# Optimization experiments

Measured on AMD Instinct MI355X. Metric: run time of the kernel, lower is better.

Reference implementation:

```python
import jax, jax.numpy as jnp
import numpy as np

ROTARY_BASE = 10000
INFTY_APPROX = 1e30
B, T, M, H, D = 2, 2048, 2048, 16, 128


def rope(x):
    # x: [B, T, H, D]; half-split rotary encoding
    *_, length, _, width = x.shape
    half = width // 2
    positions = jnp.arange(length, dtype=jnp.float32)[None, :, None, None]      # [1,T,1,1]
    dims = jnp.arange(half, dtype=jnp.float32)
    ang_freqs = jnp.power(float(ROTARY_BASE), -dims / half)[None, None, None, :]  # [1,1,1,D/2]
    radians = positions * ang_freqs
    cos = jnp.cos(radians).astype(x.dtype)
    sin = jnp.sin(radians).astype(x.dtype)
    even, odd = x[..., :half], x[..., half:]
    r_even = even * cos - odd * sin
    r_odd = even * sin + odd * cos
    return jnp.concatenate([r_even, r_odd], axis=-1)


def setup_inputs() -> dict:
    key = jax.random.key(0)
    k0, k1, k2, k3, k4 = jax.random.split(key, 5)
    return {
        "x": jax.random.normal(k0, (B, T, M), dtype=jnp.float32),
        "w_aq": jax.random.normal(k1, (H, M, D), dtype=jnp.float32) * (M ** -0.5),
        "w_ak": jax.random.normal(k2, (H, M, D), dtype=jnp.float32) * (M ** -0.5),
        "w_av": jax.random.normal(k3, (H, M, D), dtype=jnp.float32) * (M ** -0.5),
        "w_ao": jax.random.normal(k4, (H, D, M), dtype=jnp.float32) * ((2 * 24 * M) ** -0.5),
    }


def reference(x, w_aq, w_ak, w_av, w_ao):
    q = jnp.einsum("btm,hmd->bthd", x, w_aq)
    k = jnp.einsum("btm,hmd->bthd", x, w_ak)
    v = jnp.einsum("btm,hmd->bthd", x, w_av)
    q = rope(q)
    k = rope(k)
    # muP attention scaling: 1/d_head (not 1/sqrt(d_head))
    mult = (1.0 / D) ** 0.5
    s = jnp.einsum("bihd,bjhd->bhij", mult * q, mult * k)  # [B,H,T,T]
    i = jnp.arange(T)[:, None]
    j = jnp.arange(T)[None, :]
    mask = (i < j)[None, None, :, :]  # mask future positions
    s = s - jnp.asarray(INFTY_APPROX, dtype=x.dtype) * mask
    p = jax.nn.softmax(s, axis=-1)
    o = jnp.einsum("bhij,bjhd->bihd", p, v)
    r = jnp.einsum("bihd,hdm->bim", o, w_ao)
    return r
```

## Files before the change

kernel.cpp:

```cpp
#include <hip/hip_runtime.h>

#define Bb 2
#define Tt 2048
#define Mm 2048
#define Hh 16
#define Dd 128

typedef __attribute__((ext_vector_type(8))) short bf16x8;
typedef __attribute__((ext_vector_type(4))) float f32x4;
typedef __attribute__((ext_vector_type(16))) float f32x16;

__device__ __forceinline__ unsigned short f2bf(float f) {
    unsigned int u = __builtin_bit_cast(unsigned int, f);
    u += 0x7FFFu + ((u >> 16) & 1u);
    return (unsigned short)(u >> 16);
}

__device__ __forceinline__ unsigned int cvt_pk_bf16(float lo, float hi) {
    unsigned int r;
    asm("v_cvt_pk_bf16_f32 %0, %1, %2" : "=v"(r) : "v"(lo), "v"(hi));
    return r;
}

__device__ __forceinline__ float fexp2(float x) { return __builtin_amdgcn_exp2f(x); }

__device__ __forceinline__ void gld16(const void* g, void* l) {
    __builtin_amdgcn_global_load_lds(
        (const __attribute__((address_space(1))) void*)g,
        (__attribute__((address_space(3))) void*)l, 16, 0, 0);
}


__global__ __launch_bounds__(256) void cvt_x2(const float* __restrict__ x,
                                              unsigned short* __restrict__ xb2) {
    const int blk = blockIdx.x;
    const int mt = blk >> 5, kt = blk & 31;
#pragma unroll
    for (int it = 0; it < 4; ++it) {
        int s = it * 256 + threadIdx.x;
        int row = ((s >> 6) & 3) * 32 + (s & 31);
        int k = (s >> 8) * 16 + ((s >> 5) & 1) * 8;
        const float* sp = x + ((long)(mt * 128 + row)) * 2048 + kt * 64 + k;
        float4 a = *(const float4*)sp;
        float4 b = *(const float4*)(sp + 4);
        uint4 pk;
        pk.x = (unsigned int)f2bf(a.x) | ((unsigned int)f2bf(a.y) << 16);
        pk.y = (unsigned int)f2bf(a.z) | ((unsigned int)f2bf(a.w) << 16);
        pk.z = (unsigned int)f2bf(b.x) | ((unsigned int)f2bf(b.y) << 16);
        pk.w = (unsigned int)f2bf(b.z) | ((unsigned int)f2bf(b.w) << 16);
        *(uint4*)(xb2 + (((long)(mt * 32 + kt)) * 1024 + s) * 8) = pk;
    }
}

__global__ __launch_bounds__(256) void w_qkv_tile(
    const float* __restrict__ wq, const float* __restrict__ wk, const float* __restrict__ wv,
    unsigned short* __restrict__ outBase) {
    __shared__ float tile[64][132];
    const int kt = blockIdx.x;
    const int zy = blockIdx.y;
    const int which = zy >> 4, head = zy & 15;
    const float* src = (which == 0 ? wq : which == 1 ? wk : wv) + (long)head * 2048 * 128;
    const int tid = threadIdx.x;
#pragma unroll
    for (int it = 0; it < 8; ++it) {
        int f = it * 256 + tid;
        int row = f >> 5, c4 = f & 31;
        float4 v = *(const float4*)(src + (long)(kt * 64 + row) * 128 + c4 * 4);
        tile[row][c4 * 4 + 0] = v.x;
        tile[row][c4 * 4 + 1] = v.y;
        tile[row][c4 * 4 + 2] = v.z;
        tile[row][c4 * 4 + 3] = v.w;
    }
    __syncthreads();
    const int ntile = head >> 1, wn = head & 1;
    unsigned short* outp = outBase + (long)which * 4194304 +
                           ((long)(ntile * 32 + kt)) * 2048 * 8;
#pragma unroll
    for (int it = 0; it < 4; ++it) {
        int up = it * 256 + tid;
        int kk = up >> 8, nf = (up >> 6) & 3, l = up & 63;
        int il = l & 31, hl = l >> 5;
        int d = il + 64 * (nf & 1) + 32 * (nf >> 1);
        int kl = kk * 16 + hl * 8;
        uint4 pk;
        pk.x = (unsigned int)f2bf(tile[kl + 0][d]) | ((unsigned int)f2bf(tile[kl + 1][d]) << 16);
        pk.y = (unsigned int)f2bf(tile[kl + 2][d]) | ((unsigned int)f2bf(tile[kl + 3][d]) << 16);
        pk.z = (unsigned int)f2bf(tile[kl + 4][d]) | ((unsigned int)f2bf(tile[kl + 5][d]) << 16);
        pk.w = (unsigned int)f2bf(tile[kl + 6][d]) | ((unsigned int)f2bf(tile[kl + 7][d]) << 16);
        int u = kk * 512 + (wn * 4 + nf) * 64 + l;
        *(uint4*)(outp + (long)u * 8) = pk;
    }
}

__global__ __launch_bounds__(256) void transpose_cvt(const float* __restrict__ in,
                                                     unsigned short* __restrict__ out,
                                                     int rows, int cols,
                                                     long in_slab, long out_slab) {
    __shared__ float tile[32][33];
    const float* ip = in + (long)blockIdx.z * in_slab;
    unsigned short* op = out + (long)blockIdx.z * out_slab;
    int r0 = blockIdx.x * 32, c0 = blockIdx.y * 32;
    int tx = threadIdx.x & 31, ty = threadIdx.x >> 5;
#pragma unroll
    for (int j = 0; j < 32; j += 8)
        tile[ty + j][tx] = ip[(long)(r0 + ty + j) * cols + c0 + tx];
    __syncthreads();
#pragma unroll
    for (int j = 0; j < 32; j += 8)
        op[(long)(c0 + ty + j) * rows + r0 + tx] = f2bf(tile[tx][ty + j]);
}

__global__ __launch_bounds__(256) void rope_tab(float* __restrict__ cosT,
                                                float* __restrict__ sinT) {
    int idx = blockIdx.x * 256 + threadIdx.x;
    int t = idx >> 6, d = idx & 63;
    float freq = powf(10000.f, -(float)d / 64.f);
    float ang = (float)t * freq;
    sinT[idx] = sinf(ang);
    cosT[idx] = cosf(ang);
}

__global__ __launch_bounds__(256, 2) void proj_gemm4(
    const unsigned short* __restrict__ xb2,
    const unsigned short* __restrict__ wT2,
    unsigned short* __restrict__ qO,
    unsigned short* __restrict__ kO,
    unsigned short* __restrict__ vtO,
    const float* __restrict__ cosT,
    const float* __restrict__ sinT) {
    __shared__ __align__(16) char lds[49152];
    const int bm = blockIdx.x;
    const int bn = blockIdx.y;
    const int mode = bn >> 3, ntile = bn & 7;
    const unsigned short* Asrc = xb2 + ((long)bm * 32) * 1024 * 8;
    const unsigned short* Bsrc = wT2 + (long)mode * 4194304 + ((long)ntile * 32) * 2048 * 8;

    const int tid = threadIdx.x, lane = tid & 63, wave = tid >> 6;
    const int il = lane & 31, hl = lane >> 5;
    const int wm = wave >> 1, wn = wave & 1;

    f32x16 acc[2][4];
#pragma unroll
    for (int a = 0; a < 2; ++a)
#pragma unroll
        for (int b2 = 0; b2 < 4; ++b2)
#pragma unroll
            for (int e = 0; e < 16; ++e) acc[a][b2][e] = 0.f;

    for (int kt = 0; kt < 32; ++kt) {
#pragma unroll
        for (int l = 0; l < 4; ++l) {
            int s = l * 256 + tid;
            gld16(Asrc + ((long)kt * 1024 + s) * 8, lds + s * 16);
        }
#pragma unroll
        for (int l = 0; l < 8; ++l) {
            int u = l * 256 + tid;
            gld16(Bsrc + ((long)kt * 2048 + u) * 8, lds + 16384 + u * 16);
        }
        asm volatile("s_waitcnt vmcnt(0)" ::: "memory");
        __builtin_amdgcn_s_barrier();

#pragma unroll
        for (int kk = 0; kk < 4; ++kk) {
            bf16x8 af[2], bf[4];
#pragma unroll
            for (int mf = 0; mf < 2; ++mf)
                af[mf] = *(const bf16x8*)(lds + (kk * 256 + (wm * 2 + mf) * 64 + lane) * 16);
#pragma unroll
            for (int nf = 0; nf < 4; ++nf)
                bf[nf] = *(const bf16x8*)(lds + 16384 + (kk * 512 + (wn * 4 + nf) * 64 + lane) * 16);
            __builtin_amdgcn_s_setprio(1);
#pragma unroll
            for (int mf = 0; mf < 2; ++mf)
#pragma unroll
                for (int nf = 0; nf < 4; ++nf)
                    acc[mf][nf] = __builtin_amdgcn_mfma_f32_32x32x16_bf16(af[mf], bf[nf], acc[mf][nf], 0, 0, 0);
            __builtin_amdgcn_s_setprio(0);
        }
        asm volatile("" ::: "memory");
        __builtin_amdgcn_s_barrier();
    }

    const int b = bm >> 4;
    const int t0 = (bm & 15) * 128;
    const int head = ntile * 2 + wn;

    if (mode < 2) {
        const float qs = (mode == 0) ? 0.011271055f : 1.0f;
        unsigned short* outp = (mode == 0) ? qO : kO;
        long hb = ((long)(b * Hh + head)) * Tt;
#pragma unroll
        for (int mf = 0; mf < 2; ++mf)
#pragma unroll
            for (int np = 0; np < 2; ++np) {
                int d_lo = il + 32 * np;
#pragma unroll
                for (int reg = 0; reg < 16; ++reg) {
                    int r = (reg & 3) + 8 * (reg >> 2) + 4 * hl;
                    int t = t0 + wm * 64 + mf * 32 + r;
                    float c = cosT[t * 64 + d_lo], s = sinT[t * 64 + d_lo];
                    float ev = acc[mf][np * 2][reg], od = acc[mf][np * 2 + 1][reg];
                    long base = (hb + t) * Dd;
                    outp[base + d_lo]      = f2bf((ev * c - od * s) * qs);
                    outp[base + d_lo + 64] = f2bf((ev * s + od * c) * qs);
                }
            }
    } else {
        char* patch = lds + wave * 8192;
        long hdbase = ((long)(b * Hh + head)) * Dd;
#pragma unroll
        for (int mf = 0; mf < 2; ++mf) {
#pragma unroll
            for (int nf = 0; nf < 4; ++nf) {
                int dslot = nf * 32 + il;
                int swz = (dslot & 3) << 4;
#pragma unroll
                for (int qg = 0; qg < 4; ++qg) {
                    uint2 w;
                    w.x = cvt_pk_bf16(acc[mf][nf][qg * 4 + 0], acc[mf][nf][qg * 4 + 1]);
                    w.y = cvt_pk_bf16(acc[mf][nf][qg * 4 + 2], acc[mf][nf][qg * 4 + 3]);
                    *(uint2*)(patch + dslot * 64 + ((qg * 16 + hl * 8) ^ swz)) = w;
                }
            }
            __builtin_amdgcn_s_waitcnt(0);
#pragma unroll
            for (int p = 0; p < 8; ++p) {
                int dslot = p * 16 + (lane >> 2);
                int t8 = lane & 3;
                uint4 v = *(const uint4*)(patch + dslot * 64 + ((t8 * 16) ^ ((dslot & 3) << 4)));
                int ordv = dslot >> 5, il2 = dslot & 31;
                int d = il2 + 32 * (ordv >> 1) + 64 * (ordv & 1);
                int tg = t0 + wm * 64 + mf * 32 + t8 * 8;
                *(uint4*)(vtO + (hdbase + d) * Tt + tg) = v;
            }
            __builtin_amdgcn_s_waitcnt(0);
        }
    }
}

__global__ __launch_bounds__(256) void attn_kernel(
    const unsigned short* __restrict__ q,
    const unsigned short* __restrict__ k,
    const unsigned short* __restrict__ vt,
    unsigned short* __restrict__ o) {
    __shared__ __align__(16) unsigned short lds[32768];

    const int lid = (int)blockIdx.x;
    const int p = lid & 255;
    const int bh = p & 31;
    const int q0 = p >> 5;
    const int qb = (lid >> 8) ? (15 - q0) : q0;

    const int tid = threadIdx.x, lane = tid & 63, wave = tid >> 6;
    const int h = lane >> 5, iln = lane & 31;

    const unsigned short* qp = q + (long)bh * Tt * Dd;
    const unsigned short* kp = k + (long)bh * Tt * Dd;
    const unsigned short* vp = vt + (long)bh * Dd * Tt;

    const int i_g = qb * 128 + wave * 32 + iln;
    bf16x8 qf[8];
#pragma unroll
    for (int kk = 0; kk < 8; ++kk)
        qf[kk] = *(const bf16x8*)(qp + (long)i_g * Dd + kk * 16 + h * 8);

    f32x16 accO[4];
#pragma unroll
    for (int nb = 0; nb < 4; ++nb)
#pragma unroll
        for (int e = 0; e < 16; ++e) accO[nb][e] = 0.f;

    float m_r = -1e30f, l_r = 0.f;
    const int ntiles = 2 * qb + 2;

    auto stage = [&](int buf, int tix) {
        const int j0s = tix * 64;
#pragma unroll
        for (int it = 0; it < 4; ++it) {
            int f = it * 256 + tid;
            int rk = f >> 4, ck = f & 15;
            gld16(kp + ((long)(j0s + rk) * Dd + ((ck ^ (rk & 7)) << 3)),
                  (char*)lds + buf * 16384 + f * 16);
            int rv = f >> 3, cv = f & 7;
            gld16(vp + ((long)rv * Tt + j0s + ((cv ^ (rv & 7)) << 3)),
                  (char*)lds + 32768 + buf * 16384 + f * 16);
        }
    };

    stage(0, 0);

    for (int tix = 0; tix < ntiles; ++tix) {
        const int cur = tix & 1;
        const int j0 = tix * 64;
        if (tix + 1 < ntiles) {
            stage(cur ^ 1, tix + 1);
            asm volatile("s_waitcnt vmcnt(8)" ::: "memory");
        } else {
            asm volatile("s_waitcnt vmcnt(0)" ::: "memory");
        }
        __builtin_amdgcn_s_barrier();

        const char* Kb = (const char*)lds + cur * 16384;
        const char* Vb = (const char*)lds + 32768 + cur * 16384;

        f32x16 sacc[2];
#pragma unroll
        for (int mb = 0; mb < 2; ++mb)
#pragma unroll
            for (int e = 0; e < 16; ++e) sacc[mb][e] = 0.f;

        __builtin_amdgcn_s_setprio(1);
#pragma unroll
        for (int mb = 0; mb < 2; ++mb) {
            int row = mb * 32 + iln;
            const char* Kr = Kb + row * 256;
            int sw = row & 7;
#pragma unroll
            for (int kk = 0; kk < 8; ++kk) {
                bf16x8 kf = *(const bf16x8*)(Kr + 16 * ((kk * 2 + h) ^ sw));
                sacc[mb] = __builtin_amdgcn_mfma_f32_32x32x16_bf16(kf, qf[kk], sacc[mb], 0, 0, 0);
            }
        }
        __builtin_amdgcn_s_setprio(0);

        const bool domask = (j0 + 63 > qb * 128);
        if (domask) {
#pragma unroll
            for (int mb = 0; mb < 2; ++mb)
#pragma unroll
                for (int reg = 0; reg < 16; ++reg) {
                    int j = j0 + mb * 32 + (reg & 3) + 8 * (reg >> 2) + 4 * h;
                    if (j > i_g) sacc[mb][reg] = -1e30f;
                }
        }

        float red[16];
#pragma unroll
        for (int r = 0; r < 16; ++r) red[r] = fmaxf(sacc[0][r], sacc[1][r]);
#pragma unroll
        for (int s = 8; s >= 1; s >>= 1)
#pragma unroll
            for (int r = 0; r < s; ++r) red[r] = fmaxf(red[r], red[r + s]);
        float mx = fmaxf(red[0], __shfl_xor(red[0], 32, 64));

        if (__any(mx > m_r + 8.f)) {
            float mn = fmaxf(m_r, mx);
            float corr = fexp2(m_r - mn);
            m_r = mn;
            l_r *= corr;
#pragma unroll
            for (int reg = 0; reg < 16; ++reg) {
                int rrow = (reg & 3) + 8 * (reg >> 2) + 4 * h;
                float c = __shfl(corr, rrow, 64);
#pragma unroll
                for (int nb = 0; nb < 4; ++nb) accO[nb][reg] *= c;
            }
        }

        float pe[2][16];
#pragma unroll
        for (int mb = 0; mb < 2; ++mb)
#pragma unroll
            for (int r = 0; r < 16; ++r) pe[mb][r] = fexp2(sacc[mb][r] - m_r);
        float sr[16];
#pragma unroll
        for (int r = 0; r < 16; ++r) sr[r] = pe[0][r] + pe[1][r];
#pragma unroll
        for (int s = 8; s >= 1; s >>= 1)
#pragma unroll
            for (int r = 0; r < s; ++r) sr[r] += sr[r + s];
        l_r += sr[0] + __shfl_xor(sr[0], 32, 64);

        unsigned int pu[2][8];
#pragma unroll
        for (int mb = 0; mb < 2; ++mb)
#pragma unroll
            for (int t = 0; t < 8; ++t)
                pu[mb][t] = cvt_pk_bf16(pe[mb][2 * t], pe[mb][2 * t + 1]);

        unsigned int rv2[2][4];
#pragma unroll
        for (int mb = 0; mb < 2; ++mb)
#pragma unroll
            for (int u = 0; u < 4; ++u) {
                unsigned int sv = h ? pu[mb][(u & 1) + 4 * (u >> 1)]
                                    : pu[mb][2 + (u & 1) + 4 * (u >> 1)];
                rv2[mb][u] = __shfl_xor(sv, 32, 64);
            }

        __builtin_amdgcn_s_setprio(1);
#pragma unroll
        for (int kk2 = 0; kk2 < 4; ++kk2) {
            const int mb = kk2 >> 1, c2 = kk2 & 1;
            unsigned int w0 = h ? rv2[mb][2 * c2 + 0] : pu[mb][4 * c2 + 0];
            unsigned int w1 = h ? rv2[mb][2 * c2 + 1] : pu[mb][4 * c2 + 1];
            unsigned int w2 = h ? pu[mb][4 * c2 + 2] : rv2[mb][2 * c2 + 0];
            unsigned int w3 = h ? pu[mb][4 * c2 + 3] : rv2[mb][2 * c2 + 1];
            uint4 aw; aw.x = w0; aw.y = w1; aw.z = w2; aw.w = w3;
            bf16x8 af = __builtin_bit_cast(bf16x8, aw);
#pragma unroll
            for (int nb = 0; nb < 4; ++nb) {
                int d = nb * 32 + iln;
                int byte = d * 128 + 16 * ((kk2 * 2 + h) ^ (d & 7));
                bf16x8 vf = *(const bf16x8*)(Vb + byte);
                accO[nb] = __builtin_amdgcn_mfma_f32_32x32x16_bf16(af, vf, accO[nb], 0, 0, 0);
            }
        }
        __builtin_amdgcn_s_setprio(0);

        asm volatile("" ::: "memory");
        __builtin_amdgcn_s_barrier();
    }

    const int b = bh >> 4, hh = bh & 15;
    float invl = 1.f / l_r;
#pragma unroll
    for (int reg = 0; reg < 16; ++reg) {
        int rrow = (reg & 3) + 8 * (reg >> 2) + 4 * h;
        float iv = __shfl(invl, rrow, 64);
        int t = qb * 128 + wave * 32 + rrow;
        long base = ((long)(b * Tt + t) * Hh + hh) * Dd;
#pragma unroll
        for (int nb = 0; nb < 4; ++nb)
            o[base + nb * 32 + iln] = f2bf(accO[nb][reg] * iv);
    }
}

__global__ __launch_bounds__(256) void out_gemm(
    const unsigned short* __restrict__ oIn,
    const unsigned short* __restrict__ woT,
    float* __restrict__ out) {
    __shared__ __align__(16) unsigned short smem[32768];
    const int bm = blockIdx.x, bn = blockIdx.y;
    const int tid = threadIdx.x;
    const int lane = tid & 63;
    const int wave = tid >> 6;
    const int g = lane >> 4;
    const int ln = lane & 15;

    const unsigned short* arow = oIn + (long)bm * 128 * Mm;
    const unsigned short* brow = woT + (long)bn * 128 * Mm;

    f32x4 acc[2][8];
#pragma unroll
    for (int a = 0; a < 2; ++a)
#pragma unroll
        for (int b2 = 0; b2 < 8; ++b2)
#pragma unroll
            for (int e = 0; e < 4; ++e) acc[a][b2][e] = 0.f;

    auto stage = [&](int buf, int kt) {
        const int k0 = kt * 64;
#pragma unroll
        for (int it = 0; it < 4; ++it) {
            int f = it * 256 + tid;
            int r = f >> 3, c = f & 7;
            long off = (long)r * Mm + k0 + ((c ^ (r & 7)) << 3);
            gld16(arow + off, (char*)smem + buf * 32768 + f * 16);
            gld16(brow + off, (char*)smem + buf * 32768 + 16384 + f * 16);
        }
    };

    stage(0, 0);

    for (int kt = 0; kt < Mm / 64; ++kt) {
        const int cur = kt & 1;
        if (kt + 1 < Mm / 64) {
            stage(cur ^ 1, kt + 1);
            asm volatile("s_waitcnt vmcnt(8)" ::: "memory");
        } else {
            asm volatile("s_waitcnt vmcnt(0)" ::: "memory");
        }
        __builtin_amdgcn_s_barrier();

        const char* Ab = (const char*)smem + cur * 32768;
        const char* Bv = Ab + 16384;
#pragma unroll
        for (int kc = 0; kc < 2; ++kc) {
            bf16x8 af[2];
#pragma unroll
            for (int rf = 0; rf < 2; ++rf) {
                int row = wave * 32 + rf * 16 + ln;
                int byte = (row * 128 + kc * 64 + g * 16) ^ ((row & 7) << 4);
                af[rf] = *(const bf16x8*)(Ab + byte);
            }
#pragma unroll
            for (int ni = 0; ni < 8; ++ni) {
                int row = ni * 16 + ln;
                int byte = (row * 128 + kc * 64 + g * 16) ^ ((row & 7) << 4);
                bf16x8 bfv = *(const bf16x8*)(Bv + byte);
#pragma unroll
                for (int rf = 0; rf < 2; ++rf)
                    acc[rf][ni] = __builtin_amdgcn_mfma_f32_16x16x32_bf16(af[rf], bfv, acc[rf][ni], 0, 0, 0);
            }
        }
        asm volatile("" ::: "memory");
        __builtin_amdgcn_s_barrier();
    }

#pragma unroll
    for (int rf = 0; rf < 2; ++rf)
#pragma unroll
        for (int reg = 0; reg < 4; ++reg) {
            long row = bm * 128 + wave * 32 + rf * 16 + g * 4 + reg;
#pragma unroll
            for (int ni = 0; ni < 8; ++ni)
                out[row * Mm + bn * 128 + ni * 16 + ln] = acc[rf][ni][reg];
        }
}


extern "C" void kernel_launch(void* const* d_in, const int* in_sizes, int n_in,
                              void* d_out, int out_size, void* d_ws, size_t ws_size,
                              hipStream_t stream) {
    const float* x    = (const float*)d_in[0];
    const float* w_aq = (const float*)d_in[1];
    const float* w_ak = (const float*)d_in[2];
    const float* w_av = (const float*)d_in[3];
    const float* w_ao = (const float*)d_in[4];
    float* out = (float*)d_out;

    char* ws = (char*)d_ws;
    const long SZ_BTM = 16777216;
    const long SZ_W   = 8388608;
    unsigned short* xb2 = (unsigned short*)(ws);
    unsigned short* qB  = (unsigned short*)(ws + SZ_BTM);
    unsigned short* kB  = (unsigned short*)(ws + 2 * SZ_BTM);
    unsigned short* vtB = (unsigned short*)(ws + 3 * SZ_BTM);
    unsigned short* oB  = (unsigned short*)(ws + 4 * SZ_BTM);
    unsigned short* wT2 = (unsigned short*)(ws + 5 * SZ_BTM);
    unsigned short* woT = (unsigned short*)(ws + 5 * SZ_BTM + 3 * SZ_W);
    float* cosT = (float*)(ws + 5 * SZ_BTM + 4 * SZ_W);
    float* sinT = (float*)(ws + 5 * SZ_BTM + 4 * SZ_W + 524288);

    cvt_x2<<<1024, 256, 0, stream>>>(x, xb2);
    w_qkv_tile<<<dim3(32, 48), 256, 0, stream>>>(w_aq, w_ak, w_av, wT2);
    transpose_cvt<<<dim3(64, 64, 1), 256, 0, stream>>>(w_ao, woT, 2048, 2048, 0, 0);
    rope_tab<<<512, 256, 0, stream>>>(cosT, sinT);

    proj_gemm4<<<dim3(32, 24), 256, 0, stream>>>(xb2, wT2, qB, kB, vtB, cosT, sinT);
    attn_kernel<<<dim3(512), 256, 0, stream>>>(qB, kB, vtB, oB);
    out_gemm<<<dim3(32, 16), 256, 0, stream>>>(oB, woT, out);
}
```

Measured before the change: 267.9 us.

## Double-buffer LDS in QKV projection GEMM with half-size k-steps

The projection GEMM now splits each 64-wide k-tile into two halves and double-buffers them in LDS (two 24 KB buffers), issuing the next stage's global loads before waiting on the current one with a partial vmcnt. The aim is to overlap global-to-LDS traffic with MFMA work instead of serialising load then compute. Launch bounds are raised to 3 blocks per CU to allow more occupancy. The trailing barrier must still protect buffer reuse, and the higher occupancy target may add register pressure.

```diff
diff --git a/kernel.cpp b/kernel.cpp
--- a/kernel.cpp
+++ b/kernel.cpp
@@ -120,7 +120,7 @@
     cosT[idx] = cosf(ang);
 }
 
-__global__ __launch_bounds__(256, 2) void proj_gemm4(
+__global__ __launch_bounds__(256, 3) void proj_gemm5(
     const unsigned short* __restrict__ xb2,
     const unsigned short* __restrict__ wT2,
     unsigned short* __restrict__ qO,
@@ -147,29 +147,45 @@
 #pragma unroll
             for (int e = 0; e < 16; ++e) acc[a][b2][e] = 0.f;
 
-    for (int kt = 0; kt < 32; ++kt) {
+    auto stage = [&](int buf, int kt2) {
+        const int kt = kt2 >> 1, hf = kt2 & 1;
+        const unsigned short* A0 = Asrc + ((long)kt * 1024 + hf * 512) * 8;
+        const unsigned short* B0 = Bsrc + ((long)kt * 2048 + hf * 1024) * 8;
+        char* dst = lds + buf * 24576;
+#pragma unroll
+        for (int l = 0; l < 2; ++l) {
+            int s = l * 256 + tid;
+            gld16(A0 + (long)s * 8, dst + s * 16);
+        }
 #pragma unroll
         for (int l = 0; l < 4; ++l) {
-            int s = l * 256 + tid;
-            gld16(Asrc + ((long)kt * 1024 + s) * 8, lds + s * 16);
-        }
-#pragma unroll
-        for (int l = 0; l < 8; ++l) {
             int u = l * 256 + tid;
-            gld16(Bsrc + ((long)kt * 2048 + u) * 8, lds + 16384 + u * 16);
-        }
-        asm volatile("s_waitcnt vmcnt(0)" ::: "memory");
+            gld16(B0 + (long)u * 8, dst + 8192 + u * 16);
+        }
+    };
+
+    stage(0, 0);
+
+    for (int kt2 = 0; kt2 < 64; ++kt2) {
+        const int cur = kt2 & 1;
+        if (kt2 + 1 < 64) {
+            stage(cur ^ 1, kt2 + 1);
+            asm volatile("s_waitcnt vmcnt(6)" ::: "memory");
+        } else {
+            asm volatile("s_waitcnt vmcnt(0)" ::: "memory");
+        }
         __builtin_amdgcn_s_barrier();
 
-#pragma unroll
-        for (int kk = 0; kk < 4; ++kk) {
+        const char* bc = lds + cur * 24576;
+#pragma unroll
+        for (int kk2 = 0; kk2 < 2; ++kk2) {
             bf16x8 af[2], bf[4];
 #pragma unroll
             for (int mf = 0; mf < 2; ++mf)
-                af[mf] = *(const bf16x8*)(lds + (kk * 256 + (wm * 2 + mf) * 64 + lane) * 16);
+                af[mf] = *(const bf16x8*)(bc + (kk2 * 256 + (wm * 2 + mf) * 64 + lane) * 16);
 #pragma unroll
             for (int nf = 0; nf < 4; ++nf)
-                bf[nf] = *(const bf16x8*)(lds + 16384 + (kk * 512 + (wn * 4 + nf) * 64 + lane) * 16);
+                bf[nf] = *(const bf16x8*)(bc + 8192 + (kk2 * 512 + (wn * 4 + nf) * 64 + lane) * 16);
             __builtin_amdgcn_s_setprio(1);
 #pragma unroll
             for (int mf = 0; mf < 2; ++mf)
@@ -539,7 +555,7 @@
     transpose_cvt<<<dim3(64, 64, 1), 256, 0, stream>>>(w_ao, woT, 2048, 2048, 0, 0);
     rope_tab<<<512, 256, 0, stream>>>(cosT, sinT);
 
-    proj_gemm4<<<dim3(32, 24), 256, 0, stream>>>(xb2, wT2, qB, kB, vtB, cosT, sinT);
+    proj_gemm5<<<dim3(32, 24), 256, 0, stream>>>(xb2, wT2, qB, kB, vtB, cosT, sinT);
     attn_kernel<<<dim3(512), 256, 0, stream>>>(qB, kB, vtB, oB);
     out_gemm<<<dim3(32, 16), 256, 0, stream>>>(oB, woT, out);
 }
```

Measured after the change: 265.9 us. No clear change (-0.7%).

## Restructure QKV projection GEMM into 512-thread blocks with triple-buffered pipelined loads

Applied to the files above, without the earlier changes.

The QKV projection kernel is rewritten to use 512-thread blocks covering 256 rows. Each block handles a 384-column slice as one wide 256-column sub-GEMM followed by one narrow 128-column sub-GEMM, which gives a 16x16 grid of 256 blocks. The main loop now uses a three-slot LDS ring with split half-stage prefetch and partial vmcnt waits, so global loads overlap with MFMA work instead of waiting on a full drain each k-step. The weight pre-tiling layout is changed to per-head contiguous segments to match. The aim is to raise data reuse per block, cut the tail-wave imbalance, and hide load latency, at the cost of more LDS, more barriers, and a more complex schedule.

```diff
diff --git a/kernel.cpp b/kernel.cpp
--- a/kernel.cpp
+++ b/kernel.cpp
@@ -72,9 +72,7 @@
         tile[row][c4 * 4 + 3] = v.w;
     }
     __syncthreads();
-    const int ntile = head >> 1, wn = head & 1;
-    unsigned short* outp = outBase + (long)which * 4194304 +
-                           ((long)(ntile * 32 + kt)) * 2048 * 8;
+    unsigned short* outp = outBase + (((long)(which * 16 + head)) * 32 + kt) * 1024 * 8;
 #pragma unroll
     for (int it = 0; it < 4; ++it) {
         int up = it * 256 + tid;
@@ -87,8 +85,7 @@
         pk.y = (unsigned int)f2bf(tile[kl + 2][d]) | ((unsigned int)f2bf(tile[kl + 3][d]) << 16);
         pk.z = (unsigned int)f2bf(tile[kl + 4][d]) | ((unsigned int)f2bf(tile[kl + 5][d]) << 16);
         pk.w = (unsigned int)f2bf(tile[kl + 6][d]) | ((unsigned int)f2bf(tile[kl + 7][d]) << 16);
-        int u = kk * 512 + (wn * 4 + nf) * 64 + l;
-        *(uint4*)(outp + (long)u * 8) = pk;
+        *(uint4*)(outp + (long)up * 8) = pk;
     }
 }
 
@@ -120,7 +117,191 @@
     cosT[idx] = cosf(ang);
 }
 
-__global__ __launch_bounds__(256, 2) void proj_gemm4(
+template <bool WIDE>
+__device__ __forceinline__ void proj_sub(
+    const unsigned short* __restrict__ xb2,
+    const unsigned short* __restrict__ wT2,
+    char* lds, int bm, int offc,
+    unsigned short* __restrict__ qO, unsigned short* __restrict__ kO,
+    unsigned short* __restrict__ vtO,
+    const float* __restrict__ cosT, const float* __restrict__ sinT, int tid) {
+    const int lane = tid & 63, wave = tid >> 6;
+    const int il = lane & 31, hl = lane >> 5;
+    const int wm = WIDE ? (wave >> 2) : (wave >> 1);
+    const int wn = WIDE ? (wave & 3) : (wave & 1);
+    const int hseg0 = offc >> 7;
+    const int mode = offc >> 11;
+    constexpr int MF = WIDE ? 4 : 2;
+
+    f32x16 acc[MF][2];
+#pragma unroll
+    for (int a = 0; a < MF; ++a)
+#pragma unroll
+        for (int b2 = 0; b2 < 2; ++b2)
+#pragma unroll
+            for (int e = 0; e < 16; ++e) acc[a][b2][e] = 0.f;
+
+    auto stage = [&](int buf, int t, int half) {
+        const int kt = t >> 1, hf = t & 1;
+        char* dst = lds + buf * 32768;
+        if (WIDE) {
+#pragma unroll
+            for (int i = 0; i < 2; ++i) {
+                int f = (half * 2 + i) * 512 + tid;
+                if (f < 1024) {
+                    int kk = f >> 9, rf = (f >> 6) & 7, l = f & 63;
+                    int mt = 2 * bm + (rf >> 2), rb = rf & 3;
+                    gld16(xb2 + (((long)(mt * 32 + kt)) * 1024 + (2 * hf + kk) * 256 + rb * 64 + l) * 8,
+                          dst + f * 16);
+                } else {
+                    int g = f - 1024;
+                    int kk = g >> 9, cf = (g >> 6) & 7, l = g & 63;
+                    int hs = hseg0 + (cf >> 2), nf = cf & 3;
+                    gld16(wT2 + (((long)(hs * 32 + kt)) * 1024 + (2 * hf + kk) * 256 + nf * 64 + l) * 8,
+                          dst + 16384 + g * 16);
+                }
+            }
+        } else {
+            const int i0 = half ? 2 : 0, i1 = half ? 3 : 2;
+            for (int i = i0; i < i1; ++i) {
+                int f = i * 512 + tid;
+                if (f < 1024) {
+                    int kk = f >> 9, rf = (f >> 6) & 7, l = f & 63;
+                    int mt = 2 * bm + (rf >> 2), rb = rf & 3;
+                    gld16(xb2 + (((long)(mt * 32 + kt)) * 1024 + (2 * hf + kk) * 256 + rb * 64 + l) * 8,
+                          dst + f * 16);
+                } else {
+                    int g = f - 1024;
+                    int kk = g >> 8, nf = (g >> 6) & 3, l = g & 63;
+                    gld16(wT2 + (((long)(hseg0 * 32 + kt)) * 1024 + (2 * hf + kk) * 256 + nf * 64 + l) * 8,
+                          dst + 16384 + g * 16);
+                }
+            }
+        }
+    };
+
+    stage(0, 0, 0); stage(0, 0, 1);
+    stage(1, 1, 0); stage(1, 1, 1);
+
+    int cur = 0;
+    for (int t = 0; t < 64; ++t) {
+        int pre = cur + 2; if (pre >= 3) pre -= 3;
+        const char* bc = lds + cur * 32768;
+
+        if (t + 2 < 64) {
+            stage(pre, t + 2, 0);
+            if (WIDE) asm volatile("s_waitcnt vmcnt(6)" ::: "memory");
+            else      asm volatile("s_waitcnt vmcnt(5)" ::: "memory");
+        } else if (t == 62) {
+            if (WIDE) asm volatile("s_waitcnt vmcnt(4)" ::: "memory");
+            else      asm volatile("s_waitcnt vmcnt(3)" ::: "memory");
+        } else {
+            asm volatile("s_waitcnt vmcnt(0)" ::: "memory");
+        }
+        asm volatile("s_barrier" ::: "memory");
+        {
+            bf16x8 af[MF], bf[2];
+#pragma unroll
+            for (int mf = 0; mf < MF; ++mf)
+                af[mf] = *(const bf16x8*)(bc + ((wm * MF + mf) * 64 + lane) * 16);
+#pragma unroll
+            for (int nf = 0; nf < 2; ++nf)
+                bf[nf] = *(const bf16x8*)(bc + 16384 + ((wn * 2 + nf) * 64 + lane) * 16);
+            asm volatile("s_waitcnt lgkmcnt(0)" ::: "memory");
+            __builtin_amdgcn_s_setprio(1);
+#pragma unroll
+            for (int mf = 0; mf < MF; ++mf)
+#pragma unroll
+                for (int nf = 0; nf < 2; ++nf)
+                    acc[mf][nf] = __builtin_amdgcn_mfma_f32_32x32x16_bf16(af[mf], bf[nf], acc[mf][nf], 0, 0, 0);
+            __builtin_amdgcn_s_setprio(0);
+        }
+        asm volatile("s_barrier" ::: "memory");
+
+        if (t + 2 < 64) stage(pre, t + 2, 1);
+        asm volatile("s_barrier" ::: "memory");
+        {
+            constexpr int BO = WIDE ? 512 : 256;
+            bf16x8 af[MF], bf[2];
+#pragma unroll
+            for (int mf = 0; mf < MF; ++mf)
+                af[mf] = *(const bf16x8*)(bc + (512 + (wm * MF + mf) * 64 + lane) * 16);
+#pragma unroll
+            for (int nf = 0; nf < 2; ++nf)
+                bf[nf] = *(const bf16x8*)(bc + 16384 + (BO + (wn * 2 + nf) * 64 + lane) * 16);
+            asm volatile("s_waitcnt lgkmcnt(0)" ::: "memory");
+            __builtin_amdgcn_s_setprio(1);
+#pragma unroll
+            for (int mf = 0; mf < MF; ++mf)
+#pragma unroll
+                for (int nf = 0; nf < 2; ++nf)
+                    acc[mf][nf] = __builtin_amdgcn_mfma_f32_32x32x16_bf16(af[mf], bf[nf], acc[mf][nf], 0, 0, 0);
+            __builtin_amdgcn_s_setprio(0);
+        }
+        asm volatile("s_barrier" ::: "memory");
+        cur = (cur == 2) ? 0 : cur + 1;
+    }
+    asm volatile("s_waitcnt vmcnt(0)" ::: "memory");
+    __syncthreads();
+
+    const int b = bm >> 3;
+    const int t0 = (bm & 7) * 256;
+    const int head_g = WIDE ? (hseg0 + (wn >> 1)) : hseg0;
+    const int head_l = head_g & 15;
+    const int opar = WIDE ? (wn & 1) : wn;
+    constexpr int WMS = WIDE ? 128 : 64;
+
+    if (mode < 2) {
+        const float qs = (mode == 0) ? 0.011271055f : 1.0f;
+        unsigned short* outp = (mode == 0) ? qO : kO;
+        long hb = ((long)(b * Hh + head_l)) * Tt;
+        int d_lo = il + 32 * opar;
+#pragma unroll
+        for (int mf = 0; mf < MF; ++mf)
+#pragma unroll
+            for (int reg = 0; reg < 16; ++reg) {
+                int r = (reg & 3) + 8 * (reg >> 2) + 4 * hl;
+                int tt = t0 + wm * WMS + mf * 32 + r;
+                float c = cosT[tt * 64 + d_lo], s = sinT[tt * 64 + d_lo];
+                float ev = acc[mf][0][reg], od = acc[mf][1][reg];
+                long base = (hb + tt) * Dd;
+                outp[base + d_lo]      = f2bf((ev * c - od * s) * qs);
+                outp[base + d_lo + 64] = f2bf((ev * s + od * c) * qs);
+            }
+    } else {
+        char* patch = lds + wave * 4096;
+        long hdbase = ((long)(b * Hh + head_l)) * Dd * Tt;
+#pragma unroll
+        for (int mf = 0; mf < MF; ++mf) {
+#pragma unroll
+            for (int nf = 0; nf < 2; ++nf) {
+                int dslot = nf * 32 + il;
+                int swz = (dslot & 3) << 4;
+#pragma unroll
+                for (int qg = 0; qg < 4; ++qg) {
+                    uint2 w;
+                    w.x = cvt_pk_bf16(acc[mf][nf][qg * 4 + 0], acc[mf][nf][qg * 4 + 1]);
+                    w.y = cvt_pk_bf16(acc[mf][nf][qg * 4 + 2], acc[mf][nf][qg * 4 + 3]);
+                    *(uint2*)(patch + dslot * 64 + ((qg * 16 + hl * 8) ^ swz)) = w;
+                }
+            }
+            __builtin_amdgcn_s_waitcnt(0);
+#pragma unroll
+            for (int p = 0; p < 4; ++p) {
+                int dslot = p * 16 + (lane >> 2);
+                int t8 = lane & 3;
+                uint4 v = *(const uint4*)(patch + dslot * 64 + ((t8 * 16) ^ ((dslot & 3) << 4)));
+                int o = opar * 2 + (dslot >> 5), il2 = dslot & 31;
+                int dd = il2 + 32 * (o >> 1) + 64 * (o & 1);
+                int tg = t0 + wm * WMS + mf * 32 + t8 * 8;
+                *(uint4*)(vtO + hdbase + (long)dd * Tt + tg) = v;
+            }
+            __builtin_amdgcn_s_waitcnt(0);
+        }
+    }
+}
+
+__global__ __launch_bounds__(512, 2) void proj_gemm7(
     const unsigned short* __restrict__ xb2,
     const unsigned short* __restrict__ wT2,
     unsigned short* __restrict__ qO,
@@ -128,115 +309,18 @@
     unsigned short* __restrict__ vtO,
     const float* __restrict__ cosT,
     const float* __restrict__ sinT) {
-    __shared__ __align__(16) char lds[49152];
+    __shared__ __align__(16) char lds[98304];
     const int bm = blockIdx.x;
-    const int bn = blockIdx.y;
-    const int mode = bn >> 3, ntile = bn & 7;
-    const unsigned short* Asrc = xb2 + ((long)bm * 32) * 1024 * 8;
-    const unsigned short* Bsrc = wT2 + (long)mode * 4194304 + ((long)ntile * 32) * 2048 * 8;
-
-    const int tid = threadIdx.x, lane = tid & 63, wave = tid >> 6;
-    const int il = lane & 31, hl = lane >> 5;
-    const int wm = wave >> 1, wn = wave & 1;
-
-    f32x16 acc[2][4];
-#pragma unroll
-    for (int a = 0; a < 2; ++a)
-#pragma unroll
-        for (int b2 = 0; b2 < 4; ++b2)
-#pragma unroll
-            for (int e = 0; e < 16; ++e) acc[a][b2][e] = 0.f;
-
-    for (int kt = 0; kt < 32; ++kt) {
-#pragma unroll
-        for (int l = 0; l < 4; ++l) {
-            int s = l * 256 + tid;
-            gld16(Asrc + ((long)kt * 1024 + s) * 8, lds + s * 16);
-        }
-#pragma unroll
-        for (int l = 0; l < 8; ++l) {
-            int u = l * 256 + tid;
-            gld16(Bsrc + ((long)kt * 2048 + u) * 8, lds + 16384 + u * 16);
-        }
-        asm volatile("s_waitcnt vmcnt(0)" ::: "memory");
-        __builtin_amdgcn_s_barrier();
-
-#pragma unroll
-        for (int kk = 0; kk < 4; ++kk) {
-            bf16x8 af[2], bf[4];
-#pragma unroll
-            for (int mf = 0; mf < 2; ++mf)
-                af[mf] = *(const bf16x8*)(lds + (kk * 256 + (wm * 2 + mf) * 64 + lane) * 16);
-#pragma unroll
-            for (int nf = 0; nf < 4; ++nf)
-                bf[nf] = *(const bf16x8*)(lds + 16384 + (kk * 512 + (wn * 4 + nf) * 64 + lane) * 16);
-            __builtin_amdgcn_s_setprio(1);
-#pragma unroll
-            for (int mf = 0; mf < 2; ++mf)
-#pragma unroll
-                for (int nf = 0; nf < 4; ++nf)
-                    acc[mf][nf] = __builtin_amdgcn_mfma_f32_32x32x16_bf16(af[mf], bf[nf], acc[mf][nf], 0, 0, 0);
-            __builtin_amdgcn_s_setprio(0);
-        }
-        asm volatile("" ::: "memory");
-        __builtin_amdgcn_s_barrier();
-    }
-
-    const int b = bm >> 4;
-    const int t0 = (bm & 15) * 128;
-    const int head = ntile * 2 + wn;
-
-    if (mode < 2) {
-        const float qs = (mode == 0) ? 0.011271055f : 1.0f;
-        unsigned short* outp = (mode == 0) ? qO : kO;
-        long hb = ((long)(b * Hh + head)) * Tt;
-#pragma unroll
-        for (int mf = 0; mf < 2; ++mf)
-#pragma unroll
-            for (int np = 0; np < 2; ++np) {
-                int d_lo = il + 32 * np;
-#pragma unroll
-                for (int reg = 0; reg < 16; ++reg) {
-                    int r = (reg & 3) + 8 * (reg >> 2) + 4 * hl;
-                    int t = t0 + wm * 64 + mf * 32 + r;
-                    float c = cosT[t * 64 + d_lo], s = sinT[t * 64 + d_lo];
-                    float ev = acc[mf][np * 2][reg], od = acc[mf][np * 2 + 1][reg];
-                    long base = (hb + t) * Dd;
-                    outp[base + d_lo]      = f2bf((ev * c - od * s) * qs);
-                    outp[base + d_lo + 64] = f2bf((ev * s + od * c) * qs);
-                }
-            }
-    } else {
-        char* patch = lds + wave * 8192;
-        long hdbase = ((long)(b * Hh + head)) * Dd;
-#pragma unroll
-        for (int mf = 0; mf < 2; ++mf) {
-#pragma unroll
-            for (int nf = 0; nf < 4; ++nf) {
-                int dslot = nf * 32 + il;
-                int swz = (dslot & 3) << 4;
-#pragma unroll
-                for (int qg = 0; qg < 4; ++qg) {
-                    uint2 w;
-                    w.x = cvt_pk_bf16(acc[mf][nf][qg * 4 + 0], acc[mf][nf][qg * 4 + 1]);
-                    w.y = cvt_pk_bf16(acc[mf][nf][qg * 4 + 2], acc[mf][nf][qg * 4 + 3]);
-                    *(uint2*)(patch + dslot * 64 + ((qg * 16 + hl * 8) ^ swz)) = w;
-                }
-            }
-            __builtin_amdgcn_s_waitcnt(0);
-#pragma unroll
-            for (int p = 0; p < 8; ++p) {
-                int dslot = p * 16 + (lane >> 2);
-                int t8 = lane & 3;
-                uint4 v = *(const uint4*)(patch + dslot * 64 + ((t8 * 16) ^ ((dslot & 3) << 4)));
-                int ordv = dslot >> 5, il2 = dslot & 31;
-                int d = il2 + 32 * (ordv >> 1) + 64 * (ordv & 1);
-                int tg = t0 + wm * 64 + mf * 32 + t8 * 8;
-                *(uint4*)(vtO + (hdbase + d) * Tt + tg) = v;
-            }
-            __builtin_amdgcn_s_waitcnt(0);
-        }
-    }
+    const int bc = blockIdx.y;
+    const int s = bc * 384;
+    const bool swap = ((s & 2047) == 1920);
+    const int offw = swap ? s + 128 : s;
+    const int offn = swap ? s : s + 256;
+    const int tid = threadIdx.x;
+
+    proj_sub<true>(xb2, wT2, lds, bm, offw, qO, kO, vtO, cosT, sinT, tid);
+    __syncthreads();
+    proj_sub<false>(xb2, wT2, lds, bm, offn, qO, kO, vtO, cosT, sinT, tid);
 }
 
 __global__ __launch_bounds__(256) void attn_kernel(
@@ -401,8 +485,8 @@
             bf16x8 af = __builtin_bit_cast(bf16x8, aw);
 #pragma unroll
             for (int nb = 0; nb < 4; ++nb) {
-                int d = nb * 32 + iln;
-                int byte = d * 128 + 16 * ((kk2 * 2 + h) ^ (d & 7));
+                int dd = nb * 32 + iln;
+                int byte = dd * 128 + 16 * ((kk2 * 2 + h) ^ (dd & 7));
                 bf16x8 vf = *(const bf16x8*)(Vb + byte);
                 accO[nb] = __builtin_amdgcn_mfma_f32_32x32x16_bf16(af, vf, accO[nb], 0, 0, 0);
             }
@@ -539,7 +623,7 @@
     transpose_cvt<<<dim3(64, 64, 1), 256, 0, stream>>>(w_ao, woT, 2048, 2048, 0, 0);
     rope_tab<<<512, 256, 0, stream>>>(cosT, sinT);
 
-    proj_gemm4<<<dim3(32, 24), 256, 0, stream>>>(xb2, wT2, qB, kB, vtB, cosT, sinT);
+    proj_gemm7<<<dim3(16, 16), 512, 0, stream>>>(xb2, wT2, qB, kB, vtB, cosT, sinT);
     attn_kernel<<<dim3(512), 256, 0, stream>>>(qB, kB, vtB, oB);
     out_gemm<<<dim3(32, 16), 256, 0, stream>>>(oB, woT, out);
 }
```

Result: faster. 262.0 us (-2.2%).
